# Kernel tuning notes

Hardware: AMD Instinct MI355X
Metric: run time of the kernel (lower is better)

## Reference

```python
import jax, jax.numpy as jnp
import numpy as np

B, NUM_FRAMES, NUM_PATCHES = 2, 16, 196
DIM, H, DH = 768, 12, 64
T = NUM_FRAMES * NUM_PATCHES  # 3136
EPS = 1e-5


def setup_inputs() -> dict:
    key = jax.random.key(0)
    ks = jax.random.split(key, 5)
    x = jax.random.normal(ks[0], (B, T, DIM), jnp.float32)
    context = jax.random.normal(ks[1], (B, T, DIM), jnp.float32)
    Wq = jax.random.normal(ks[2], (DIM, H * DH), jnp.float32) * 0.02
    Wkv = jax.random.normal(ks[3], (DIM, 2 * H * DH), jnp.float32) * 0.02
    Wo = jax.random.normal(ks[4], (H * DH, DIM), jnp.float32) * 0.02
    bo = jnp.zeros((DIM,), jnp.float32)
    gamma = jnp.ones((DIM,), jnp.float32)
    beta = jnp.zeros((DIM,), jnp.float32)
    # block-diagonal frame mask: patch i attends to patch j iff same frame
    frame_ids = jnp.arange(T) // NUM_PATCHES
    mask = frame_ids[:, None] == frame_ids[None, :]  # [T, T] bool
    return {"x": x, "context": context, "Wq": Wq, "Wkv": Wkv, "Wo": Wo,
            "bo": bo, "gamma": gamma, "beta": beta, "mask": mask}


def reference(x, context, Wq, Wkv, Wo, bo, gamma, beta, mask):
    # LayerNorm on queries only (torch LN: biased variance, eps=1e-5)
    mu = jnp.mean(x, axis=-1, keepdims=True)
    var = jnp.var(x, axis=-1, keepdims=True)
    xn = (x - mu) * jax.lax.rsqrt(var + EPS) * gamma + beta

    q = xn @ Wq                      # [B, T, H*DH]
    kv = context @ Wkv               # [B, T, 2*H*DH]
    k, v = jnp.split(kv, 2, axis=-1)

    def split_heads(t):
        return t.reshape(B, T, H, DH).transpose(0, 2, 1, 3)  # [B, H, T, DH]

    q, k, v = split_heads(q), split_heads(k), split_heads(v)

    scale = DH ** -0.5
    dots = jnp.einsum('bhnd,bhmd->bhnm', q, k) * scale      # [B, H, T, T]
    dots = jnp.where(mask, dots, -jnp.inf)
    attn = jax.nn.softmax(dots, axis=-1)                    # dropout p=0.0 -> identity
    out = jnp.einsum('bhnm,bhmd->bhnd', attn, v)            # [B, H, T, DH]
    out = out.transpose(0, 2, 1, 3).reshape(B, T, H * DH)
    return out @ Wo + bo
```

## Files before the change

kernel.cpp:

```cpp
#include <hip/hip_runtime.h>
#include <hip/hip_bf16.h>

#define NB 2
#define TT 3136
#define DIM 768
#define NH 12
#define NF 16
#define NP 196

typedef __attribute__((ext_vector_type(8))) short short8;
typedef __attribute__((ext_vector_type(4))) short s16x4;
typedef __attribute__((ext_vector_type(4))) float f32x4;
typedef unsigned int uint;

__device__ __forceinline__ float bf2f(short s) {
    return __uint_as_float(((uint)(unsigned short)s) << 16);
}
__device__ __forceinline__ short f2bs(float f) {
    __hip_bfloat16 h = __float2bfloat16(f);
    short s; __builtin_memcpy(&s, &h, 2); return s;
}
__device__ __forceinline__ void load16_lds(const void* g, void* l) {
    __builtin_amdgcn_global_load_lds(
        (const __attribute__((address_space(1))) unsigned int*)g,
        (__attribute__((address_space(3))) unsigned int*)l, 16, 0, 0);
}

__global__ __launch_bounds__(256)
void prep_w(const float* __restrict__ Wq, const float* __restrict__ Wkv,
            const float* __restrict__ Wo,
            __hip_bfloat16* __restrict__ WqT, __hip_bfloat16* __restrict__ WkvT,
            __hip_bfloat16* __restrict__ WoT) {
    __shared__ float tile[32][33];
    int bx = blockIdx.x;
    const float* W; __hip_bfloat16* WT; int N, n0;
    if (bx < 24)      { W = Wq;  WT = WqT;  N = DIM;     n0 = bx * 32; }
    else if (bx < 72) { W = Wkv; WT = WkvT; N = 2 * DIM; n0 = (bx - 24) * 32; }
    else              { W = Wo;  WT = WoT;  N = DIM;     n0 = (bx - 72) * 32; }
    int k0 = blockIdx.y * 32;
    int tx = threadIdx.x & 31, ty = threadIdx.x >> 5;
#pragma unroll
    for (int i = 0; i < 32; i += 8)
        tile[ty + i][tx] = W[(size_t)(k0 + ty + i) * N + (n0 + tx)];
    __syncthreads();
#pragma unroll
    for (int i = 0; i < 32; i += 8)
        WT[(size_t)(n0 + ty + i) * DIM + (k0 + tx)] = __float2bfloat16(tile[tx][ty + i]);
}

__global__ __launch_bounds__(256)
void prep_xc(const float* __restrict__ ctx, __hip_bfloat16* __restrict__ cb,
             const float* __restrict__ x, const float* __restrict__ gamma,
             const float* __restrict__ beta, __hip_bfloat16* __restrict__ xn) {
    int blk = blockIdx.x, tid = threadIdx.x;
    if (blk < 4704) {
        size_t i = (size_t)blk * 256 + tid;
        f32x4 f; __builtin_memcpy(&f, ctx + i * 4, 16);
        s16x4 s;
#pragma unroll
        for (int j = 0; j < 4; j++) s[j] = f2bs(f[j]);
        __builtin_memcpy((short*)cb + i * 4, &s, 8);
        return;
    }
    int row = blk - 4704;
    const float* xr = x + (size_t)row * DIM;
    float v[3], s = 0.f, ss = 0.f;
#pragma unroll
    for (int i = 0; i < 3; i++) {
        v[i] = xr[tid + i * 256];
        s += v[i]; ss += v[i] * v[i];
    }
#pragma unroll
    for (int off = 32; off; off >>= 1) {
        s += __shfl_xor(s, off);
        ss += __shfl_xor(ss, off);
    }
    __shared__ float red[8];
    int wid = tid >> 6, lane = tid & 63;
    if (lane == 0) { red[wid] = s; red[wid + 4] = ss; }
    __syncthreads();
    if (tid == 0) {
        float S = red[0] + red[1] + red[2] + red[3];
        float SS = red[4] + red[5] + red[6] + red[7];
        float mu = S / DIM;
        float var = SS / DIM - mu * mu;
        red[0] = mu;
        red[1] = rsqrtf(var + 1e-5f);
    }
    __syncthreads();
    float mu = red[0], rs = red[1];
#pragma unroll
    for (int i = 0; i < 3; i++) {
        int c = tid + i * 256;
        xn[(size_t)row * DIM + c] = __float2bfloat16((v[i] - mu) * rs * gamma[c] + beta[c]);
    }
}

__global__ __launch_bounds__(256)
void gemm_qkv(const __hip_bfloat16* __restrict__ xn,
              const __hip_bfloat16* __restrict__ cb,
              const __hip_bfloat16* __restrict__ WqT,
              const __hip_bfloat16* __restrict__ WkvT,
              __hip_bfloat16* __restrict__ qbuf,
              __hip_bfloat16* __restrict__ kvbuf) {
    __shared__ short sA[128 * 64];
    __shared__ short sB[128 * 64];
    int y = blockIdx.y;
    const __hip_bfloat16 *A, *BT;
    __hip_bfloat16* C;
    int N, n0;
    if (y < 6) { A = xn; BT = WqT;  C = qbuf;  N = DIM;     n0 = y * 128; }
    else       { A = cb; BT = WkvT; C = kvbuf; N = 2 * DIM; n0 = (y - 6) * 128; }
    int m0 = blockIdx.x * 128;
    int tid = threadIdx.x, lane = tid & 63, wave = tid >> 6;
    int r = lane & 15, q = lane >> 4;
    int wm = (wave & 1) * 64, wn = (wave >> 1) * 64;
    f32x4 acc[4][4] = {};
    for (int k0 = 0; k0 < DIM; k0 += 64) {
#pragma unroll
        for (int i = 0; i < 4; i++) {
            int c = i * 256 + tid;
            int row = c >> 3, cg = c & 7;
            load16_lds(A + (size_t)(m0 + row) * DIM + k0 + cg * 8, &sA[c * 8]);
        }
#pragma unroll
        for (int i = 0; i < 4; i++) {
            int c = i * 256 + tid;
            int row = c >> 3, cg = c & 7;
            load16_lds(BT + (size_t)(n0 + row) * DIM + k0 + cg * 8, &sB[c * 8]);
        }
        __syncthreads();
#pragma unroll
        for (int ks = 0; ks < 2; ks++) {
            short8 af[4], bf[4];
#pragma unroll
            for (int t = 0; t < 4; t++) {
                __builtin_memcpy(&af[t], &sA[(wm + t * 16 + r) * 64 + ks * 32 + q * 8], 16);
                __builtin_memcpy(&bf[t], &sB[(wn + t * 16 + r) * 64 + ks * 32 + q * 8], 16);
            }
#pragma unroll
            for (int mi = 0; mi < 4; mi++)
#pragma unroll
                for (int ni = 0; ni < 4; ni++)
                    acc[mi][ni] = __builtin_amdgcn_mfma_f32_16x16x32_bf16(
                        af[mi], bf[ni], acc[mi][ni], 0, 0, 0);
        }
        __syncthreads();
    }
#pragma unroll
    for (int mi = 0; mi < 4; mi++)
#pragma unroll
        for (int ni = 0; ni < 4; ni++)
#pragma unroll
            for (int rr = 0; rr < 4; rr++) {
                int row = m0 + wm + mi * 16 + q * 4 + rr;
                int col = n0 + wn + ni * 16 + r;
                C[(size_t)row * N + col] = __float2bfloat16(acc[mi][ni][rr]);
            }
}

__global__ __launch_bounds__(256)
void gemm_o(const __hip_bfloat16* __restrict__ A,
            const __hip_bfloat16* __restrict__ BT,
            const float* __restrict__ bias,
            float* __restrict__ C) {
    __shared__ short sA[128 * 64];
    __shared__ short sB[128 * 64];
    int m0 = blockIdx.x * 128, n0 = blockIdx.y * 128;
    int tid = threadIdx.x, lane = tid & 63, wave = tid >> 6;
    int r = lane & 15, q = lane >> 4;
    int wm = (wave & 1) * 64, wn = (wave >> 1) * 64;
    f32x4 acc[4][4] = {};
    for (int k0 = 0; k0 < DIM; k0 += 64) {
#pragma unroll
        for (int i = 0; i < 4; i++) {
            int c = i * 256 + tid;
            int row = c >> 3, cg = c & 7;
            load16_lds(A + (size_t)(m0 + row) * DIM + k0 + cg * 8, &sA[c * 8]);
        }
#pragma unroll
        for (int i = 0; i < 4; i++) {
            int c = i * 256 + tid;
            int row = c >> 3, cg = c & 7;
            load16_lds(BT + (size_t)(n0 + row) * DIM + k0 + cg * 8, &sB[c * 8]);
        }
        __syncthreads();
#pragma unroll
        for (int ks = 0; ks < 2; ks++) {
            short8 af[4], bf[4];
#pragma unroll
            for (int t = 0; t < 4; t++) {
                __builtin_memcpy(&af[t], &sA[(wm + t * 16 + r) * 64 + ks * 32 + q * 8], 16);
                __builtin_memcpy(&bf[t], &sB[(wn + t * 16 + r) * 64 + ks * 32 + q * 8], 16);
            }
#pragma unroll
            for (int mi = 0; mi < 4; mi++)
#pragma unroll
                for (int ni = 0; ni < 4; ni++)
                    acc[mi][ni] = __builtin_amdgcn_mfma_f32_16x16x32_bf16(
                        af[mi], bf[ni], acc[mi][ni], 0, 0, 0);
        }
        __syncthreads();
    }
    float bv[4];
#pragma unroll
    for (int ni = 0; ni < 4; ni++) bv[ni] = bias[n0 + wn + ni * 16 + r];
#pragma unroll
    for (int mi = 0; mi < 4; mi++)
#pragma unroll
        for (int ni = 0; ni < 4; ni++)
#pragma unroll
            for (int rr = 0; rr < 4; rr++) {
                int row = m0 + wm + mi * 16 + q * 4 + rr;
                int col = n0 + wn + ni * 16 + r;
                C[(size_t)row * DIM + col] = acc[mi][ni][rr] + bv[ni];
            }
}

__global__ __launch_bounds__(448)
void attn_kernel(__hip_bfloat16* qo,
                 const __hip_bfloat16* __restrict__ kvb) {
    __shared__ short sQ[112 * 66];
    __shared__ short sK[208 * 66];
    __shared__ short sVT[64 * 226];
    int blk = blockIdx.x;
    int half = blk & 1;
    int rest = blk >> 1;
    int f = rest % NF, h = (rest / NF) % NH, b = rest / (NF * NH);
    size_t tok0 = (size_t)b * TT + (size_t)f * NP;
    int row0 = half * 98;
    int tid = threadIdx.x, wave = tid >> 6, lane = tid & 63;
    int r = lane & 15, q = lane >> 4;

    for (int e = tid; e < 896; e += 448) {
        int row = e >> 3, cg = e & 7;
        short8 t = {0,0,0,0,0,0,0,0};
        if (row < 98)
            __builtin_memcpy(&t, qo + (tok0 + row0 + row) * DIM + h * 64 + cg * 8, 16);
        __builtin_memcpy(&sQ[row * 66 + cg * 8], &t, 16);
    }
    for (int e = tid; e < 1664; e += 448) {
        int row = e >> 3, cg = e & 7;
        short8 t = {0,0,0,0,0,0,0,0};
        if (row < NP)
            __builtin_memcpy(&t, kvb + (tok0 + row) * 1536 + h * 64 + cg * 8, 16);
        __builtin_memcpy(&sK[row * 66 + cg * 8], &t, 16);
    }
    for (int jj = 0; jj < 224; jj += 28) {
        int j = jj + (tid >> 4);
        int d = (tid & 15) * 4;
        s16x4 v = {0, 0, 0, 0};
        if (j < NP)
            __builtin_memcpy(&v, kvb + (tok0 + j) * 1536 + DIM + h * 64 + d, 8);
#pragma unroll
        for (int i = 0; i < 4; i++) sVT[(d + i) * 226 + j] = v[i];
    }
    __syncthreads();

    f32x4 sacc[13];
    short8 qf0, qf1;
    __builtin_memcpy(&qf0, &sQ[(wave * 16 + r) * 66 + q * 8], 16);
    __builtin_memcpy(&qf1, &sQ[(wave * 16 + r) * 66 + 32 + q * 8], 16);
#pragma unroll
    for (int jf = 0; jf < 13; jf++) {
        f32x4 a = {};
        short8 kf;
        __builtin_memcpy(&kf, &sK[(jf * 16 + r) * 66 + q * 8], 16);
        a = __builtin_amdgcn_mfma_f32_16x16x32_bf16(kf, qf0, a, 0, 0, 0);
        __builtin_memcpy(&kf, &sK[(jf * 16 + r) * 66 + 32 + q * 8], 16);
        a = __builtin_amdgcn_mfma_f32_16x16x32_bf16(kf, qf1, a, 0, 0, 0);
        sacc[jf] = a;
    }

    const float scale = 0.125f;
    float mx = -INFINITY;
#pragma unroll
    for (int jf = 0; jf < 13; jf++)
#pragma unroll
        for (int rg = 0; rg < 4; rg++) {
            bool valid = (jf < 12) | (q == 0);
            if (valid) mx = fmaxf(mx, sacc[jf][rg] * scale);
        }
    mx = fmaxf(mx, __shfl_xor(mx, 16));
    mx = fmaxf(mx, __shfl_xor(mx, 32));
    float ps = 0.f;
#pragma unroll
    for (int jf = 0; jf < 13; jf++)
#pragma unroll
        for (int rg = 0; rg < 4; rg++) {
            bool valid = (jf < 12) | (q == 0);
            float p = valid ? __expf(sacc[jf][rg] * scale - mx) : 0.f;
            sacc[jf][rg] = p;
            ps += p;
        }
    ps += __shfl_xor(ps, 16);
    ps += __shfl_xor(ps, 32);
    float inv = 1.f / ps;

    int srcl[8];
#pragma unroll
    for (int e = 0; e < 8; e++)
        srcl[e] = ((((q * 8 + e) >> 2) & 3) << 4) | r;
    short8 pa[7];
#pragma unroll
    for (int c = 0; c < 7; c++) {
#pragma unroll
        for (int e = 0; e < 8; e++) {
            float v0 = __shfl(sacc[2 * c][e & 3], srcl[e], 64);
            float v1 = (c < 6) ? __shfl(sacc[2 * c + 1][e & 3], srcl[e], 64) : 0.f;
            float val = (q >= 2) ? v1 : v0;
            pa[c][e] = f2bs(val * inv);
        }
    }

#pragma unroll
    for (int nt = 0; nt < 4; nt++) {
        f32x4 oacc = {};
#pragma unroll
        for (int kc = 0; kc < 7; kc++) {
            short8 bfv;
            __builtin_memcpy(&bfv, &sVT[(nt * 16 + r) * 226 + kc * 32 + q * 8], 16);
            oacc = __builtin_amdgcn_mfma_f32_16x16x32_bf16(pa[kc], bfv, oacc, 0, 0, 0);
        }
#pragma unroll
        for (int rg = 0; rg < 4; rg++) {
            int local = wave * 16 + q * 4 + rg;
            if (local < 98)
                qo[(tok0 + row0 + local) * DIM + h * 64 + nt * 16 + r] =
                    __float2bfloat16(oacc[rg]);
        }
    }
}

extern "C" void kernel_launch(void* const* d_in, const int* in_sizes, int n_in,
                              void* d_out, int out_size, void* d_ws, size_t ws_size,
                              hipStream_t stream) {
    const float* x     = (const float*)d_in[0];
    const float* ctx   = (const float*)d_in[1];
    const float* Wq    = (const float*)d_in[2];
    const float* Wkv   = (const float*)d_in[3];
    const float* Wo    = (const float*)d_in[4];
    const float* bo    = (const float*)d_in[5];
    const float* gamma = (const float*)d_in[6];
    const float* beta  = (const float*)d_in[7];

    char* ws = (char*)d_ws;
    __hip_bfloat16* cbuf  = (__hip_bfloat16*)(ws + 0);
    __hip_bfloat16* kvbuf = (__hip_bfloat16*)(ws + 9633792);
    __hip_bfloat16* qbuf  = (__hip_bfloat16*)(ws + 28901376);
    __hip_bfloat16* WqT   = (__hip_bfloat16*)(ws + 38535168);
    __hip_bfloat16* WkvT  = (__hip_bfloat16*)(ws + 39714816);
    __hip_bfloat16* WoT   = (__hip_bfloat16*)(ws + 42074112);
    __hip_bfloat16* xnbuf = (__hip_bfloat16*)d_out;
    float*          out   = (float*)d_out;

    prep_w<<<dim3(96, 24), 256, 0, stream>>>(Wq, Wkv, Wo, WqT, WkvT, WoT);
    prep_xc<<<10976, 256, 0, stream>>>(ctx, cbuf, x, gamma, beta, xnbuf);
    gemm_qkv<<<dim3(49, 18), 256, 0, stream>>>(xnbuf, cbuf, WqT, WkvT, qbuf, kvbuf);
    attn_kernel<<<NB * NH * NF * 2, 448, 0, stream>>>(qbuf, kvbuf);
    gemm_o<<<dim3(49, 6), 256, 0, stream>>>(qbuf, WoT, bo, out);
}
```

Baseline: 220.0 us.

## Double-buffer LDS in projection GEMMs, remap blocks per XCD, raise MFMA priority

Both projection GEMMs now stage the next K tile into a second LDS buffer while MFMAs run on the current one, halving the barriers per iteration. Launches become 1D, and block IDs are remapped so consecutive tiles land on the same XCD for better L2 reuse. s_setprio raises wave priority around the MFMA bursts. LDS use doubles to 64KB per block, which may reduce occupancy.

```diff
diff --git a/kernel.cpp b/kernel.cpp
--- a/kernel.cpp
+++ b/kernel.cpp
@@ -103,50 +103,69 @@
               const __hip_bfloat16* __restrict__ WkvT,
               __hip_bfloat16* __restrict__ qbuf,
               __hip_bfloat16* __restrict__ kvbuf) {
-    __shared__ short sA[128 * 64];
-    __shared__ short sB[128 * 64];
-    int y = blockIdx.y;
+    __shared__ short sA[2][128 * 64];
+    __shared__ short sB[2][128 * 64];
+    int orig = blockIdx.x;
+    int xcd = orig & 7, pos = orig >> 3;
+    int wgid = (xcd < 2 ? xcd * 111 : 222 + (xcd - 2) * 110) + pos;
+    int mt = wgid / 18, nt = wgid - mt * 18;
     const __hip_bfloat16 *A, *BT;
     __hip_bfloat16* C;
     int N, n0;
-    if (y < 6) { A = xn; BT = WqT;  C = qbuf;  N = DIM;     n0 = y * 128; }
-    else       { A = cb; BT = WkvT; C = kvbuf; N = 2 * DIM; n0 = (y - 6) * 128; }
-    int m0 = blockIdx.x * 128;
+    if (nt < 6) { A = xn; BT = WqT;  C = qbuf;  N = DIM;     n0 = nt * 128; }
+    else        { A = cb; BT = WkvT; C = kvbuf; N = 2 * DIM; n0 = (nt - 6) * 128; }
+    int m0 = mt * 128;
     int tid = threadIdx.x, lane = tid & 63, wave = tid >> 6;
     int r = lane & 15, q = lane >> 4;
     int wm = (wave & 1) * 64, wn = (wave >> 1) * 64;
     f32x4 acc[4][4] = {};
-    for (int k0 = 0; k0 < DIM; k0 += 64) {
+
+    auto stage = [&](int buf, int k0) {
 #pragma unroll
         for (int i = 0; i < 4; i++) {
             int c = i * 256 + tid;
             int row = c >> 3, cg = c & 7;
-            load16_lds(A + (size_t)(m0 + row) * DIM + k0 + cg * 8, &sA[c * 8]);
+            load16_lds(A + (size_t)(m0 + row) * DIM + k0 + cg * 8, &sA[buf][c * 8]);
         }
 #pragma unroll
         for (int i = 0; i < 4; i++) {
             int c = i * 256 + tid;
             int row = c >> 3, cg = c & 7;
-            load16_lds(BT + (size_t)(n0 + row) * DIM + k0 + cg * 8, &sB[c * 8]);
-        }
-        __syncthreads();
+            load16_lds(BT + (size_t)(n0 + row) * DIM + k0 + cg * 8, &sB[buf][c * 8]);
+        }
+    };
+    auto compute = [&](int buf) {
 #pragma unroll
         for (int ks = 0; ks < 2; ks++) {
-            short8 af[4], bf[4];
+            short8 af[4], bfv[4];
 #pragma unroll
             for (int t = 0; t < 4; t++) {
-                __builtin_memcpy(&af[t], &sA[(wm + t * 16 + r) * 64 + ks * 32 + q * 8], 16);
-                __builtin_memcpy(&bf[t], &sB[(wn + t * 16 + r) * 64 + ks * 32 + q * 8], 16);
+                __builtin_memcpy(&af[t],  &sA[buf][(wm + t * 16 + r) * 64 + ks * 32 + q * 8], 16);
+                __builtin_memcpy(&bfv[t], &sB[buf][(wn + t * 16 + r) * 64 + ks * 32 + q * 8], 16);
             }
+            __builtin_amdgcn_s_setprio(1);
 #pragma unroll
             for (int mi = 0; mi < 4; mi++)
 #pragma unroll
                 for (int ni = 0; ni < 4; ni++)
                     acc[mi][ni] = __builtin_amdgcn_mfma_f32_16x16x32_bf16(
-                        af[mi], bf[ni], acc[mi][ni], 0, 0, 0);
-        }
+                        af[mi], bfv[ni], acc[mi][ni], 0, 0, 0);
+            __builtin_amdgcn_s_setprio(0);
+        }
+    };
+
+    stage(0, 0);
+    __syncthreads();
+    int cur = 0;
+#pragma unroll 2
+    for (int t = 0; t < 11; ++t) {
+        stage(cur ^ 1, (t + 1) * 64);
+        compute(cur);
         __syncthreads();
-    }
+        cur ^= 1;
+    }
+    compute(cur);
+
 #pragma unroll
     for (int mi = 0; mi < 4; mi++)
 #pragma unroll
@@ -164,44 +183,64 @@
             const __hip_bfloat16* __restrict__ BT,
             const float* __restrict__ bias,
             float* __restrict__ C) {
-    __shared__ short sA[128 * 64];
-    __shared__ short sB[128 * 64];
-    int m0 = blockIdx.x * 128, n0 = blockIdx.y * 128;
+    __shared__ short sA[2][128 * 64];
+    __shared__ short sB[2][128 * 64];
+    int orig = blockIdx.x;
+    int xcd = orig & 7, pos = orig >> 3;
+    int wgid = (xcd < 6 ? xcd * 37 : 222 + (xcd - 6) * 36) + pos;
+    int mt = wgid / 6, nt = wgid - mt * 6;
+    int m0 = mt * 128, n0 = nt * 128;
     int tid = threadIdx.x, lane = tid & 63, wave = tid >> 6;
     int r = lane & 15, q = lane >> 4;
     int wm = (wave & 1) * 64, wn = (wave >> 1) * 64;
     f32x4 acc[4][4] = {};
-    for (int k0 = 0; k0 < DIM; k0 += 64) {
+
+    auto stage = [&](int buf, int k0) {
 #pragma unroll
         for (int i = 0; i < 4; i++) {
             int c = i * 256 + tid;
             int row = c >> 3, cg = c & 7;
-            load16_lds(A + (size_t)(m0 + row) * DIM + k0 + cg * 8, &sA[c * 8]);
+            load16_lds(A + (size_t)(m0 + row) * DIM + k0 + cg * 8, &sA[buf][c * 8]);
         }
 #pragma unroll
         for (int i = 0; i < 4; i++) {
             int c = i * 256 + tid;
             int row = c >> 3, cg = c & 7;
-            load16_lds(BT + (size_t)(n0 + row) * DIM + k0 + cg * 8, &sB[c * 8]);
-        }
-        __syncthreads();
+            load16_lds(BT + (size_t)(n0 + row) * DIM + k0 + cg * 8, &sB[buf][c * 8]);
+        }
+    };
+    auto compute = [&](int buf) {
 #pragma unroll
         for (int ks = 0; ks < 2; ks++) {
-            short8 af[4], bf[4];
+            short8 af[4], bfv[4];
 #pragma unroll
             for (int t = 0; t < 4; t++) {
-                __builtin_memcpy(&af[t], &sA[(wm + t * 16 + r) * 64 + ks * 32 + q * 8], 16);
-                __builtin_memcpy(&bf[t], &sB[(wn + t * 16 + r) * 64 + ks * 32 + q * 8], 16);
+                __builtin_memcpy(&af[t],  &sA[buf][(wm + t * 16 + r) * 64 + ks * 32 + q * 8], 16);
+                __builtin_memcpy(&bfv[t], &sB[buf][(wn + t * 16 + r) * 64 + ks * 32 + q * 8], 16);
             }
+            __builtin_amdgcn_s_setprio(1);
 #pragma unroll
             for (int mi = 0; mi < 4; mi++)
 #pragma unroll
                 for (int ni = 0; ni < 4; ni++)
                     acc[mi][ni] = __builtin_amdgcn_mfma_f32_16x16x32_bf16(
-                        af[mi], bf[ni], acc[mi][ni], 0, 0, 0);
-        }
+                        af[mi], bfv[ni], acc[mi][ni], 0, 0, 0);
+            __builtin_amdgcn_s_setprio(0);
+        }
+    };
+
+    stage(0, 0);
+    __syncthreads();
+    int cur = 0;
+#pragma unroll 2
+    for (int t = 0; t < 11; ++t) {
+        stage(cur ^ 1, (t + 1) * 64);
+        compute(cur);
         __syncthreads();
-    }
+        cur ^= 1;
+    }
+    compute(cur);
+
     float bv[4];
 #pragma unroll
     for (int ni = 0; ni < 4; ni++) bv[ni] = bias[n0 + wn + ni * 16 + r];
@@ -356,7 +395,7 @@
 
     prep_w<<<dim3(96, 24), 256, 0, stream>>>(Wq, Wkv, Wo, WqT, WkvT, WoT);
     prep_xc<<<10976, 256, 0, stream>>>(ctx, cbuf, x, gamma, beta, xnbuf);
-    gemm_qkv<<<dim3(49, 18), 256, 0, stream>>>(xnbuf, cbuf, WqT, WkvT, qbuf, kvbuf);
+    gemm_qkv<<<882, 256, 0, stream>>>(xnbuf, cbuf, WqT, WkvT, qbuf, kvbuf);
     attn_kernel<<<NB * NH * NF * 2, 448, 0, stream>>>(qbuf, kvbuf);
-    gemm_o<<<dim3(49, 6), 256, 0, stream>>>(qbuf, WoT, bo, out);
-}
+    gemm_o<<<294, 256, 0, stream>>>(qbuf, WoT, bo, out);
+}
```

Result: faster. 205.3 us (-6.7%).
